# Kernel optimization log

Measured on AMD Instinct MI355X. Metric: run time of the kernel, lower is better.

The kernel has to match this reference:

```python
import jax, jax.numpy as jnp
import numpy as np

H = 256          # LSTM hidden size
P = 1            # proj_size
L = 5            # num LSTM layers
T = 1000         # sequence length (forced by Linear(1000, 100))


def _uniform(key, shape, scale):
    return jax.random.uniform(key, shape, dtype=jnp.float32, minval=-scale, maxval=scale)


def setup_inputs() -> dict:
    key = jax.random.key(0)
    ks = jax.random.split(key, 16)
    B = 128
    s = 1.0 / np.sqrt(H)  # PyTorch LSTM init scale
    inp = {
        "x": jax.random.normal(ks[0], (B, T, 1), dtype=jnp.float32),
        # stacked LSTM params: layer input dim is 1 for all layers (input_size=1, proj_size=1)
        "Wih": _uniform(ks[1], (L, 4 * H, 1), s),
        "Whh": _uniform(ks[2], (L, 4 * H, P), s),
        "bih": _uniform(ks[3], (L, 4 * H), s),
        "bhh": _uniform(ks[4], (L, 4 * H), s),
        "Whr": _uniform(ks[5], (L, P, H), s),
        # MLP head
        "W1": _uniform(ks[6], (100, 1000), 1.0 / np.sqrt(1000)),
        "b1": _uniform(ks[7], (100,), 1.0 / np.sqrt(1000)),
        "W2": _uniform(ks[8], (100, 100), 0.1),
        "b2": _uniform(ks[9], (100,), 0.1),
        "W3": _uniform(ks[10], (100, 100), 0.1),
        "b3": _uniform(ks[11], (100,), 0.1),
        "W4": _uniform(ks[12], (1, 100), 0.1),
        "b4": _uniform(ks[13], (1,), 0.1),
    }
    return inp


def _lstm_layer(x_seq, Wih, Whh, bih, bhh, Whr):
    """One projected LSTM layer. x_seq: [B, T, in_dim] -> [B, T, P]."""
    B = x_seq.shape[0]
    # precompute input contribution for all timesteps: [B, T, 4H]
    gx = jnp.einsum('bti,gi->btg', x_seq, Wih) + bih + bhh
    gx = jnp.transpose(gx, (1, 0, 2))  # [T, B, 4H] for scan

    def step(carry, g_t):
        h, c = carry                      # h: [B, P], c: [B, H]
        gates = g_t + h @ Whh.T           # [B, 4H]
        i = jax.nn.sigmoid(gates[:, 0 * H:1 * H])
        f = jax.nn.sigmoid(gates[:, 1 * H:2 * H])
        g = jnp.tanh(gates[:, 2 * H:3 * H])
        o = jax.nn.sigmoid(gates[:, 3 * H:4 * H])
        c = f * c + i * g
        h = (o * jnp.tanh(c)) @ Whr.T     # projected hidden: [B, P]
        return (h, c), h

    h0 = jnp.zeros((B, P), x_seq.dtype)
    c0 = jnp.zeros((B, H), x_seq.dtype)
    _, hs = jax.lax.scan(step, (h0, c0), gx)  # hs: [T, B, P]
    return jnp.transpose(hs, (1, 0, 2))       # [B, T, P]


def reference(x, Wih, Whh, bih, bhh, Whr, W1, b1, W2, b2, W3, b3, W4, b4):
    out = x
    for l in range(L):  # fixed 5 stacked layers
        out = _lstm_layer(out, Wih[l], Whh[l], bih[l], bhh[l], Whr[l])
    out = out[:, :, 0]                      # squeeze -> [B, 1000]
    out = jax.nn.sigmoid(out @ W1.T + b1)   # linear1 + Sigmoid
    out = jax.nn.sigmoid(out @ W2.T + b2)   # linear2 + Sigmoid
    out = jax.nn.relu(out @ W3.T + b3)      # linear3 + ReLU
    out = out @ W4.T + b4                   # linear4 -> [B, 1]
    return out
```

## Files before the change

### kernel.cpp

```cpp
#include <hip/hip_runtime.h>


#define HSZ 256
#define LAYERS 5
#define TT 1000
#define BATCH 128

__device__ __forceinline__ float fast_exp2(float x) {
#if __has_builtin(__builtin_amdgcn_exp2f)
  return __builtin_amdgcn_exp2f(x);
#else
  return __exp2f(x);
#endif
}
__device__ __forceinline__ float fast_rcp(float x) {
#if __has_builtin(__builtin_amdgcn_rcpf)
  return __builtin_amdgcn_rcpf(x);
#else
  return 1.0f / x;
#endif
}
__device__ __forceinline__ float fast_sigmoid(float z) {
  float e = fast_exp2(-1.4426950408889634f * z);
  return fast_rcp(1.0f + e);
}
__device__ __forceinline__ float fast_tanh(float z) {
  float e = fast_exp2(-2.8853900817779268f * z);
  return fmaf(2.0f, fast_rcp(1.0f + e), -1.0f);
}

template <int CTRL>
__device__ __forceinline__ float dpp_add(float v) {
  int moved = __builtin_amdgcn_update_dpp(0, __builtin_bit_cast(int, v),
                                          CTRL, 0xF, 0xF, false);
  return v + __builtin_bit_cast(float, moved);
}

__device__ __forceinline__ float wave_sum(float v) {
  v = dpp_add<0x128>(v);
  v = dpp_add<0x124>(v);
  v = dpp_add<0x122>(v);
  v = dpp_add<0x121>(v);
  int sw = __builtin_amdgcn_ds_swizzle(__builtin_bit_cast(int, v), 0x401F);
  v = v + __builtin_bit_cast(float, sw);
  float lo = __builtin_bit_cast(float, __builtin_amdgcn_readlane(__builtin_bit_cast(int, v), 0));
  float hi = __builtin_bit_cast(float, __builtin_amdgcn_readlane(__builtin_bit_cast(int, v), 32));
  return lo + hi;
}

__global__ __launch_bounds__(512) void lstm_pipeline_kernel(
    const float* __restrict__ x,
    const float* __restrict__ Wih,
    const float* __restrict__ Whh,
    const float* __restrict__ bih,
    const float* __restrict__ bhh,
    const float* __restrict__ Whr,
    float* __restrict__ seq_out)
{
  __shared__ float xs[TT];
  __shared__ float part[2][4];
  __shared__ __align__(16) float part4[2][4];

  const int b    = blockIdx.x;
  const int tid  = threadIdx.x;
  const int wave = tid >> 6;
  const int lane = tid & 63;
  const bool big = (wave < 4);
  const int layer = big ? wave : 4;
  const int nq    = wave - 4;

  for (int i = tid; i < TT; i += 512) xs[i] = x[b * TT + i];
  if (tid < 8) { ((float*)part)[tid] = 0.0f; ((float*)part4)[tid] = 0.0f; }

  float wi[4][4], wh[4][4], bs[4][4], whr[4], c[4];
  const int base = layer * 1024;
  if (big) {
#pragma unroll
    for (int g = 0; g < 4; ++g)
#pragma unroll
      for (int k = 0; k < 4; ++k) {
        int j = base + g * 256 + k * 64 + lane;
        wi[g][k] = Wih[j];
        wh[g][k] = Whh[j];
        bs[g][k] = bih[j] + bhh[j];
      }
#pragma unroll
    for (int k = 0; k < 4; ++k) {
      whr[k] = Whr[layer * 256 + k * 64 + lane];
      c[k] = 0.0f;
    }
  } else {
#pragma unroll
    for (int g = 0; g < 4; ++g) {
      int j = base + g * 256 + nq * 64 + lane;
      wi[g][0] = Wih[j];
      wh[g][0] = Whh[j];
      bs[g][0] = bih[j] + bhh[j];
#pragma unroll
      for (int k = 1; k < 4; ++k) { wi[g][k] = 0.f; wh[g][k] = 0.f; bs[g][k] = 0.f; }
    }
    whr[0] = Whr[4 * 256 + nq * 64 + lane];
#pragma unroll
    for (int k = 0; k < 4; ++k) c[k] = 0.0f;
#pragma unroll
    for (int k = 1; k < 4; ++k) whr[k] = 0.0f;
  }
  float h_own = 0.0f;
  __syncthreads();

  auto cell = [&](int k, float x_in) -> float {
    float pi = fmaf(x_in, wi[0][k], fmaf(h_own, wh[0][k], bs[0][k]));
    float pf = fmaf(x_in, wi[1][k], fmaf(h_own, wh[1][k], bs[1][k]));
    float pg = fmaf(x_in, wi[2][k], fmaf(h_own, wh[2][k], bs[2][k]));
    float po = fmaf(x_in, wi[3][k], fmaf(h_own, wh[3][k], bs[3][k]));
    float ig = fast_sigmoid(pi);
    float fg = fast_sigmoid(pf);
    float gg = fast_tanh(pg);
    float og = fast_sigmoid(po);
    c[k] = fmaf(fg, c[k], ig * gg);
    return og * fast_tanh(c[k]) * whr[k];
  };

  for (int it = 0; it < TT + LAYERS; ++it) {
    const int p  = it & 1;
    const int p1 = (it - 1) & 1;
    const int t  = it - layer;

    if (!big) {
      float4 q = *(const float4*)&part4[p1][0];
      h_own = (q.x + q.y) + (q.z + q.w);
      if (nq == 0 && lane == 0) {
        int tp = it - 1 - 4;
        if (tp >= 0 && tp < TT) seq_out[b * TT + tp] = h_own;
      }
    }

    const bool active = (t >= 0) && (t < TT);
    if (active) {
      float x_in = (layer == 0) ? xs[t]
                 : (big ? part[p1][layer - 1] : part[p1][3]);
      float r;
      if (big) {
        r = 0.0f;
#pragma unroll
        for (int k = 0; k < 4; ++k) r += cell(k, x_in);
      } else {
        r = cell(0, x_in);
      }
      r = wave_sum(r);
      if (big) {
        h_own = r;
        if (lane == 0) part[p][layer] = r;
      } else {
        if (lane == 0) part4[p][nq] = r;
      }
    }
    __syncthreads();
  }
}

__global__ __launch_bounds__(128) void mlp_head_kernel(
    const float* __restrict__ seq,
    const float* __restrict__ W1, const float* __restrict__ b1,
    const float* __restrict__ W2, const float* __restrict__ b2,
    const float* __restrict__ W3, const float* __restrict__ b3,
    const float* __restrict__ W4, const float* __restrict__ b4,
    float* __restrict__ out)
{
  __shared__ float sx[TT];
  __shared__ float sh[100];
  __shared__ float sh2[100];
  __shared__ float red[2];

  const int b = blockIdx.x, tid = threadIdx.x;
  for (int i = tid; i < TT; i += 128) sx[i] = seq[b * TT + i];
  __syncthreads();

  if (tid < 100) {
    float acc = b1[tid];
    const float* w = W1 + tid * TT;
    for (int t0 = 0; t0 < TT; t0 += 4) {
      float4 v = *(const float4*)(w + t0);
      acc += v.x * sx[t0 + 0];
      acc += v.y * sx[t0 + 1];
      acc += v.z * sx[t0 + 2];
      acc += v.w * sx[t0 + 3];
    }
    sh[tid] = fast_sigmoid(acc);
  }
  __syncthreads();

  if (tid < 100) {
    float acc = b2[tid];
    const float* w = W2 + tid * 100;
    for (int k = 0; k < 100; ++k) acc += w[k] * sh[k];
    sh2[tid] = fast_sigmoid(acc);
  }
  __syncthreads();

  if (tid < 100) {
    float acc = b3[tid];
    const float* w = W3 + tid * 100;
    for (int k = 0; k < 100; ++k) acc += w[k] * sh2[k];
    sh[tid] = fmaxf(acc, 0.0f);
  }
  __syncthreads();

  float r = (tid < 100) ? sh[tid] * W4[tid] : 0.0f;
  r = wave_sum(r);
  if ((tid & 63) == 0) red[tid >> 6] = r;
  __syncthreads();
  if (tid == 0) out[b] = red[0] + red[1] + b4[0];
}

extern "C" void kernel_launch(void* const* d_in, const int* in_sizes, int n_in,
                              void* d_out, int out_size, void* d_ws, size_t ws_size,
                              hipStream_t stream) {
  const float* x   = (const float*)d_in[0];
  const float* Wih = (const float*)d_in[1];
  const float* Whh = (const float*)d_in[2];
  const float* bih = (const float*)d_in[3];
  const float* bhh = (const float*)d_in[4];
  const float* Whr = (const float*)d_in[5];
  const float* W1  = (const float*)d_in[6];
  const float* b1  = (const float*)d_in[7];
  const float* W2  = (const float*)d_in[8];
  const float* b2  = (const float*)d_in[9];
  const float* W3  = (const float*)d_in[10];
  const float* b3  = (const float*)d_in[11];
  const float* W4  = (const float*)d_in[12];
  const float* b4  = (const float*)d_in[13];

  float* seq = (float*)d_ws;

  lstm_pipeline_kernel<<<BATCH, 512, 0, stream>>>(x, Wih, Whh, bih, bhh, Whr, seq);
  mlp_head_kernel<<<BATCH, 128, 0, stream>>>(seq, W1, b1, W2, b2, W3, b3, W4, b4,
                                             (float*)d_out);
}
```

Baseline: 690.4 us.

## Split LSTM layers into separate single-wave blocks pipelined via global flags

Replaces the per-batch 512-thread block, which synchronized all layers with __syncthreads every timestep, with 640 single-wave blocks, one per (layer, batch). Each block streams 40-step chunks through global memory and signals the next layer through release/acquire flags, so no block-wide barrier sits on the recurrence critical path. Layer 4 now does full 256-wide cells in one wave instead of being split across four waves. It relies on all 640 blocks being co-resident so the spin-waits do not deadlock, and it adds pipeline fill latency per chunk plus a memset. The MLP head also gets split accumulators in its first matvec.

```diff
diff --git a/kernel.cpp b/kernel.cpp
--- a/kernel.cpp
+++ b/kernel.cpp
@@ -1,10 +1,11 @@
 #include <hip/hip_runtime.h>
 
 
-#define HSZ 256
 #define LAYERS 5
 #define TT 1000
 #define BATCH 128
+#define CH 40
+#define NCH (TT / CH)
 
 __device__ __forceinline__ float fast_exp2(float x) {
 #if __has_builtin(__builtin_amdgcn_exp2f)
@@ -48,119 +49,100 @@
   return lo + hi;
 }
 
-__global__ __launch_bounds__(512) void lstm_pipeline_kernel(
+__device__ __forceinline__ float lane_bcast(float v, int s) {
+  return __builtin_bit_cast(float, __builtin_amdgcn_readlane(__builtin_bit_cast(int, v), s));
+}
+
+__global__ __launch_bounds__(64) void lstm_wave_kernel(
     const float* __restrict__ x,
     const float* __restrict__ Wih,
     const float* __restrict__ Whh,
     const float* __restrict__ bih,
     const float* __restrict__ bhh,
     const float* __restrict__ Whr,
-    float* __restrict__ seq_out)
+    float* __restrict__ seq,
+    int* __restrict__ flags)
 {
-  __shared__ float xs[TT];
-  __shared__ float part[2][4];
-  __shared__ __align__(16) float part4[2][4];
-
-  const int b    = blockIdx.x;
-  const int tid  = threadIdx.x;
-  const int wave = tid >> 6;
-  const int lane = tid & 63;
-  const bool big = (wave < 4);
-  const int layer = big ? wave : 4;
-  const int nq    = wave - 4;
-
-  for (int i = tid; i < TT; i += 512) xs[i] = x[b * TT + i];
-  if (tid < 8) { ((float*)part)[tid] = 0.0f; ((float*)part4)[tid] = 0.0f; }
-
-  float wi[4][4], wh[4][4], bs[4][4], whr[4], c[4];
-  const int base = layer * 1024;
-  if (big) {
-#pragma unroll
-    for (int g = 0; g < 4; ++g)
+  const int bid  = blockIdx.x;
+  const int l    = bid >> 7;
+  const int b    = bid & 127;
+  const int lane = threadIdx.x;
+
+  float wi[4][4], wh[4][4], bs[4][4], whr[4], cc[4];
+  const int base = l * 1024;
+#pragma unroll
+  for (int g = 0; g < 4; ++g)
+#pragma unroll
+    for (int k = 0; k < 4; ++k) {
+      int j = base + g * 256 + k * 64 + lane;
+      wi[g][k] = Wih[j];
+      wh[g][k] = Whh[j];
+      bs[g][k] = bih[j] + bhh[j];
+    }
+#pragma unroll
+  for (int k = 0; k < 4; ++k) {
+    whr[k] = Whr[l * 256 + k * 64 + lane];
+    cc[k] = 0.0f;
+  }
+
+  const float* in  = (l == 0) ? (x + b * TT) : (seq + ((l - 1) * BATCH + b) * TT);
+  float*       out = seq + (l * BATCH + b) * TT;
+  int*       my_flag = flags + l * BATCH + b;
+  const int* in_flag = (l > 0) ? (flags + (l - 1) * BATCH + b) : (const int*)flags;
+
+  float h = 0.0f;
+  for (int c = 0; c < NCH; ++c) {
+    if (l > 0) {
+      while (__hip_atomic_load(in_flag, __ATOMIC_ACQUIRE,
+                               __HIP_MEMORY_SCOPE_AGENT) <= c)
+        __builtin_amdgcn_s_sleep(2);
+    }
+    float xv = 0.0f;
+    if (lane < CH) {
+      if (l == 0)
+        xv = in[c * CH + lane];
+      else
+        xv = __hip_atomic_load(in + c * CH + lane, __ATOMIC_RELAXED,
+                               __HIP_MEMORY_SCOPE_AGENT);
+    }
+
+    float outv = 0.0f;
+    for (int s = 0; s < CH; ++s) {
+      const float xs = lane_bcast(xv, s);
+      float r = 0.0f;
 #pragma unroll
       for (int k = 0; k < 4; ++k) {
-        int j = base + g * 256 + k * 64 + lane;
-        wi[g][k] = Wih[j];
-        wh[g][k] = Whh[j];
-        bs[g][k] = bih[j] + bhh[j];
-      }
-#pragma unroll
-    for (int k = 0; k < 4; ++k) {
-      whr[k] = Whr[layer * 256 + k * 64 + lane];
-      c[k] = 0.0f;
-    }
-  } else {
-#pragma unroll
-    for (int g = 0; g < 4; ++g) {
-      int j = base + g * 256 + nq * 64 + lane;
-      wi[g][0] = Wih[j];
-      wh[g][0] = Whh[j];
-      bs[g][0] = bih[j] + bhh[j];
-#pragma unroll
-      for (int k = 1; k < 4; ++k) { wi[g][k] = 0.f; wh[g][k] = 0.f; bs[g][k] = 0.f; }
-    }
-    whr[0] = Whr[4 * 256 + nq * 64 + lane];
-#pragma unroll
-    for (int k = 0; k < 4; ++k) c[k] = 0.0f;
-#pragma unroll
-    for (int k = 1; k < 4; ++k) whr[k] = 0.0f;
-  }
-  float h_own = 0.0f;
-  __syncthreads();
-
-  auto cell = [&](int k, float x_in) -> float {
-    float pi = fmaf(x_in, wi[0][k], fmaf(h_own, wh[0][k], bs[0][k]));
-    float pf = fmaf(x_in, wi[1][k], fmaf(h_own, wh[1][k], bs[1][k]));
-    float pg = fmaf(x_in, wi[2][k], fmaf(h_own, wh[2][k], bs[2][k]));
-    float po = fmaf(x_in, wi[3][k], fmaf(h_own, wh[3][k], bs[3][k]));
-    float ig = fast_sigmoid(pi);
-    float fg = fast_sigmoid(pf);
-    float gg = fast_tanh(pg);
-    float og = fast_sigmoid(po);
-    c[k] = fmaf(fg, c[k], ig * gg);
-    return og * fast_tanh(c[k]) * whr[k];
-  };
-
-  for (int it = 0; it < TT + LAYERS; ++it) {
-    const int p  = it & 1;
-    const int p1 = (it - 1) & 1;
-    const int t  = it - layer;
-
-    if (!big) {
-      float4 q = *(const float4*)&part4[p1][0];
-      h_own = (q.x + q.y) + (q.z + q.w);
-      if (nq == 0 && lane == 0) {
-        int tp = it - 1 - 4;
-        if (tp >= 0 && tp < TT) seq_out[b * TT + tp] = h_own;
-      }
-    }
-
-    const bool active = (t >= 0) && (t < TT);
-    if (active) {
-      float x_in = (layer == 0) ? xs[t]
-                 : (big ? part[p1][layer - 1] : part[p1][3]);
-      float r;
-      if (big) {
-        r = 0.0f;
-#pragma unroll
-        for (int k = 0; k < 4; ++k) r += cell(k, x_in);
-      } else {
-        r = cell(0, x_in);
+        float pi = fmaf(xs, wi[0][k], fmaf(h, wh[0][k], bs[0][k]));
+        float pf = fmaf(xs, wi[1][k], fmaf(h, wh[1][k], bs[1][k]));
+        float pg = fmaf(xs, wi[2][k], fmaf(h, wh[2][k], bs[2][k]));
+        float po = fmaf(xs, wi[3][k], fmaf(h, wh[3][k], bs[3][k]));
+        float ig = fast_sigmoid(pi);
+        float fg = fast_sigmoid(pf);
+        float gg = fast_tanh(pg);
+        float og = fast_sigmoid(po);
+        cc[k] = fmaf(fg, cc[k], ig * gg);
+        r += og * fast_tanh(cc[k]) * whr[k];
       }
       r = wave_sum(r);
-      if (big) {
-        h_own = r;
-        if (lane == 0) part[p][layer] = r;
-      } else {
-        if (lane == 0) part4[p][nq] = r;
-      }
-    }
-    __syncthreads();
+      h = r;
+      outv = (lane == s) ? r : outv;
+    }
+
+    if (l < 4) {
+      if (lane < CH)
+        __hip_atomic_store(out + c * CH + lane, outv, __ATOMIC_RELAXED,
+                           __HIP_MEMORY_SCOPE_AGENT);
+      if (lane == 0)
+        __hip_atomic_store(my_flag, c + 1, __ATOMIC_RELEASE,
+                           __HIP_MEMORY_SCOPE_AGENT);
+    } else {
+      if (lane < CH) out[c * CH + lane] = outv;
+    }
   }
 }
 
 __global__ __launch_bounds__(128) void mlp_head_kernel(
-    const float* __restrict__ seq,
+    const float* __restrict__ seq4,
     const float* __restrict__ W1, const float* __restrict__ b1,
     const float* __restrict__ W2, const float* __restrict__ b2,
     const float* __restrict__ W3, const float* __restrict__ b3,
@@ -173,20 +155,20 @@
   __shared__ float red[2];
 
   const int b = blockIdx.x, tid = threadIdx.x;
-  for (int i = tid; i < TT; i += 128) sx[i] = seq[b * TT + i];
+  for (int i = tid; i < TT; i += 128) sx[i] = seq4[b * TT + i];
   __syncthreads();
 
   if (tid < 100) {
-    float acc = b1[tid];
     const float* w = W1 + tid * TT;
+    float a0 = 0.f, a1 = 0.f, a2 = 0.f, a3 = 0.f;
     for (int t0 = 0; t0 < TT; t0 += 4) {
       float4 v = *(const float4*)(w + t0);
-      acc += v.x * sx[t0 + 0];
-      acc += v.y * sx[t0 + 1];
-      acc += v.z * sx[t0 + 2];
-      acc += v.w * sx[t0 + 3];
-    }
-    sh[tid] = fast_sigmoid(acc);
+      a0 = fmaf(v.x, sx[t0 + 0], a0);
+      a1 = fmaf(v.y, sx[t0 + 1], a1);
+      a2 = fmaf(v.z, sx[t0 + 2], a2);
+      a3 = fmaf(v.w, sx[t0 + 3], a3);
+    }
+    sh[tid] = fast_sigmoid((a0 + a1) + (a2 + a3) + b1[tid]);
   }
   __syncthreads();
 
@@ -207,7 +189,17 @@
   __syncthreads();
 
   float r = (tid < 100) ? sh[tid] * W4[tid] : 0.0f;
-  r = wave_sum(r);
+  {
+    r = dpp_add<0x128>(r);
+    r = dpp_add<0x124>(r);
+    r = dpp_add<0x122>(r);
+    r = dpp_add<0x121>(r);
+    int sw = __builtin_amdgcn_ds_swizzle(__builtin_bit_cast(int, r), 0x401F);
+    r = r + __builtin_bit_cast(float, sw);
+    float lo = __builtin_bit_cast(float, __builtin_amdgcn_readlane(__builtin_bit_cast(int, r), 0));
+    float hi = __builtin_bit_cast(float, __builtin_amdgcn_readlane(__builtin_bit_cast(int, r), 32));
+    r = lo + hi;
+  }
   if ((tid & 63) == 0) red[tid >> 6] = r;
   __syncthreads();
   if (tid == 0) out[b] = red[0] + red[1] + b4[0];
@@ -231,9 +223,13 @@
   const float* W4  = (const float*)d_in[12];
   const float* b4  = (const float*)d_in[13];
 
-  float* seq = (float*)d_ws;
-
-  lstm_pipeline_kernel<<<BATCH, 512, 0, stream>>>(x, Wih, Whh, bih, bhh, Whr, seq);
-  mlp_head_kernel<<<BATCH, 128, 0, stream>>>(seq, W1, b1, W2, b2, W3, b3, W4, b4,
+  float* seq   = (float*)d_ws;
+  int*   flags = (int*)(seq + LAYERS * BATCH * TT);
+
+  hipMemsetAsync(flags, 0, LAYERS * BATCH * sizeof(int), stream);
+  lstm_wave_kernel<<<LAYERS * BATCH, 64, 0, stream>>>(x, Wih, Whh, bih, bhh, Whr,
+                                                      seq, flags);
+  mlp_head_kernel<<<BATCH, 128, 0, stream>>>(seq + 4 * BATCH * TT,
+                                             W1, b1, W2, b2, W3, b3, W4, b4,
                                              (float*)d_out);
 }
```

Result: faster. 625.6 us (-9.4%).
